# Kernel optimization log

Measured on AMD Instinct MI355X. Metric: run time of the kernel, lower is better.

The kernel has to match this reference:

```python
import jax, jax.numpy as jnp
import numpy as np
import math

EMBED = 1024
HEADS = 16
B, S = 2, 1024

def setup_inputs() -> dict:
    key = jax.random.key(0)
    ks = jax.random.split(key, 6)
    sc = 1.0 / math.sqrt(EMBED)
    return {
        "x": jax.random.normal(ks[0], (B, S, EMBED), dtype=jnp.float32),
        "Wq": jax.random.normal(ks[1], (EMBED, EMBED), dtype=jnp.float32) * sc,
        "Wk": jax.random.normal(ks[2], (EMBED, EMBED), dtype=jnp.float32) * sc,
        "Wv": jax.random.normal(ks[3], (EMBED, EMBED), dtype=jnp.float32) * sc,
        "Wo": jax.random.normal(ks[4], (EMBED, EMBED), dtype=jnp.float32) * sc,
        "bo": jax.random.normal(ks[5], (EMBED,), dtype=jnp.float32) * sc,
        "heads": HEADS,
    }

def reference(x, Wq, Wk, Wv, Wo, bo, heads):
    nB, nS, nE = x.shape
    nH = heads
    nG = nE // nH  # effective number of 'heads' in this (quirky) module

    def split(W):
        # (B,S,E) -> (B,S,G,H) -> (B,G,S,H); per-head dim is nH (as in source)
        return (x @ W).reshape(nB, nS, nG, nH).transpose(0, 2, 1, 3)

    q, k, v = split(Wq), split(Wk), split(Wv)
    # scale uses k.size(-1) == heads, matching the source
    att = jnp.einsum('bgsh,bgth->bgst', q, k) / math.sqrt(nH)
    causal = jnp.tril(jnp.ones((nS, nS), dtype=bool))  # True = keep
    att = jnp.where(causal, att, -jnp.inf)
    att = jax.nn.softmax(att, axis=-1)
    y = jnp.einsum('bgst,bgth->bgsh', att, v)
    y = y.transpose(0, 2, 1, 3).reshape(nB, nS, nE)
    return y @ Wo + bo
```

## Files before the change

### kernel.cpp

```cpp
#include <hip/hip_runtime.h>
#include <hip/hip_bf16.h>
#include <stdint.h>

typedef __attribute__((ext_vector_type(8))) short bf16x8;
typedef __attribute__((ext_vector_type(4))) short bf16x4;
typedef __attribute__((ext_vector_type(4))) float f32x4;

#define NB 2
#define SEQ 1024
#define EMB 1024
#define NH 16
#define NG 64

#if defined(__has_builtin)
#if __has_builtin(__builtin_amdgcn_mfma_f32_16x16x16bf16_1k)
#define QK_1K 1
#else
#define QK_1K 0
#endif
#if __has_builtin(__builtin_amdgcn_exp2f)
#define EXP2(x) __builtin_amdgcn_exp2f(x)
#else
#define EXP2(x) exp2f(x)
#endif
#if __has_builtin(__builtin_amdgcn_rcpf)
#define RCP(x) __builtin_amdgcn_rcpf(x)
#else
#define RCP(x) (1.0f / (x))
#endif
#else
#define QK_1K 0
#define EXP2(x) exp2f(x)
#define RCP(x) (1.0f / (x))
#endif

__device__ __forceinline__ unsigned short f2bf(float f){
  uint32_t u = __float_as_uint(f);
  uint32_t r = (u + 0x7fffu + ((u >> 16) & 1u)) >> 16;
  return (unsigned short)r;
}

__device__ __forceinline__ uint32_t pack_bf2(float lo, float hi){
  uint32_t a = (__float_as_uint(lo) + 0x8000u) >> 16;
  uint32_t b = (__float_as_uint(hi) + 0x8000u) & 0xffff0000u;
  return a | b;
}

__device__ __forceinline__ void gld_lds16(const void* g, void* l){
  __builtin_amdgcn_global_load_lds((__attribute__((address_space(1))) void*)(uintptr_t)(g),
                                   (__attribute__((address_space(3))) void*)(l),
                                   16, 0, 0);
}


__global__ __launch_bounds__(256) void prep_kernel(
    const float* __restrict__ x,
    const float* __restrict__ W0, const float* __restrict__ W1,
    const float* __restrict__ W2, const float* __restrict__ W3,
    unsigned short* __restrict__ xb,
    unsigned short* __restrict__ wtAll)
{
  const int bid = blockIdx.x;
  if (bid < 2048){
    int i = (bid * 256 + threadIdx.x) * 4;
    float4 f = *(const float4*)(x + i);
    ushort4 o;
    o.x = f2bf(f.x); o.y = f2bf(f.y); o.z = f2bf(f.z); o.w = f2bf(f.w);
    *(ushort4*)(xb + i) = o;
    return;
  }
  __shared__ float tile[32][33];
  const int b2 = bid - 2048;
  const int z = b2 & 3;
  const int rest = b2 >> 2;
  const float* W = (z == 0) ? W0 : (z == 1) ? W1 : (z == 2) ? W2 : W3;
  unsigned short* o = wtAll + (size_t)z * EMB * EMB;
  const int n0 = (rest & 31) * 32, k0 = (rest >> 5) * 32;
  const int tx = threadIdx.x & 31, ty = threadIdx.x >> 5;
#pragma unroll
  for (int i = 0; i < 4; i++)
    tile[ty + 8*i][tx] = W[(size_t)(k0 + ty + 8*i) * EMB + n0 + tx];
  __syncthreads();
#pragma unroll
  for (int i = 0; i < 4; i++)
    o[(size_t)(n0 + ty + 8*i) * EMB + k0 + tx] = f2bf(tile[tx][ty + 8*i]);
}


template<int J>
__device__ __forceinline__ void stage_tile(const unsigned short* __restrict__ src,
                                           unsigned short* __restrict__ dst,
                                           int row0, int k0, int t){
#pragma unroll
  for (int j = 0; j < J; ++j){
    const int c = t + 256 * j;
    const int row = c >> 3;
    const int col8 = (c & 7) ^ (row & 7);
    gld_lds16(src + (size_t)(row0 + row) * 1024 + k0 + col8 * 8, dst + c * 8);
  }
}


__global__ __launch_bounds__(256) void gemm_qkv_kernel(
    const unsigned short* __restrict__ A,
    const unsigned short* __restrict__ WtAll,
    unsigned short* __restrict__ qws,
    unsigned short* __restrict__ kws,
    unsigned short* __restrict__ vws)
{
  __shared__ unsigned short As[2][128][64];
  __shared__ unsigned short Bs[2][64][64];
  const int z = blockIdx.z;
  const unsigned short* Bp = WtAll + (size_t)z * EMB * EMB;
  const int m0 = blockIdx.x * 128, n0 = blockIdx.y * 64;
  const int t = threadIdx.x;
  const int l = t & 63, w = t >> 6;
  const int wr = w >> 1, wc = w & 1;
  const int lr = l & 15, lk = l >> 4;
  const int sw0 = (lk ^ (lr & 7)) * 8;
  const int sw1 = ((lk + 4) ^ (lr & 7)) * 8;

  f32x4 acc[4][2];
#pragma unroll
  for (int m = 0; m < 4; m++)
#pragma unroll
    for (int n = 0; n < 2; n++)
#pragma unroll
      for (int r = 0; r < 4; r++) acc[m][n][r] = 0.f;

  stage_tile<4>(A, &As[0][0][0], m0, 0, t);
  stage_tile<2>(Bp, &Bs[0][0][0], n0, 0, t);
  __syncthreads();
  int cur = 0;
  for (int kt = 0; kt < 16; ++kt){
    if (kt < 15){
      stage_tile<4>(A, &As[cur ^ 1][0][0], m0, (kt + 1) * 64, t);
      stage_tile<2>(Bp, &Bs[cur ^ 1][0][0], n0, (kt + 1) * 64, t);
    }
#pragma unroll
    for (int half = 0; half < 2; ++half){
      const int sw = half ? sw1 : sw0;
      bf16x8 af[4], bfr[2];
#pragma unroll
      for (int m = 0; m < 4; m++) af[m]  = *(const bf16x8*)(&As[cur][wr*64 + m*16 + lr][sw]);
#pragma unroll
      for (int n = 0; n < 2; n++) bfr[n] = *(const bf16x8*)(&Bs[cur][wc*32 + n*16 + lr][sw]);
#pragma unroll
      for (int m = 0; m < 4; m++)
#pragma unroll
        for (int n = 0; n < 2; n++)
          acc[m][n] = __builtin_amdgcn_mfma_f32_16x16x32_bf16(af[m], bfr[n], acc[m][n], 0, 0, 0);
    }
    __syncthreads();
    cur ^= 1;
  }

#pragma unroll
  for (int m = 0; m < 4; m++){
    const int rowb = m0 + wr*64 + m*16 + lk*4;
#pragma unroll
    for (int n = 0; n < 2; n++){
      const int col = n0 + wc*32 + n*16 + lr;
      const int g = col >> 4, h = col & 15;
#pragma unroll
      for (int r = 0; r < 4; r++){
        const int rr = rowb + r;
        const int b = rr >> 10, s = rr & 1023;
        const int bg = b * NG + g;
        const float v = acc[m][n][r];
        if (z == 0)      qws[((size_t)bg * 1024 + s) * 16 + h] = f2bf(v * 0.36067376022f);
        else if (z == 1) kws[((size_t)bg * 1024 + s) * 16 + h] = f2bf(v);
        else             vws[((size_t)bg * 16 + h) * 1024 + s] = f2bf(v);
      }
    }
  }
}


__global__ __launch_bounds__(256) void gemm_out_kernel(
    const unsigned short* __restrict__ A,
    const unsigned short* __restrict__ Bw,
    const float* __restrict__ bo,
    float* __restrict__ out)
{
  __shared__ unsigned short As[2][64][64];
  __shared__ unsigned short Bs[2][64][64];
  const int m0 = blockIdx.x * 64, n0 = blockIdx.y * 64;
  const int t = threadIdx.x;
  const int l = t & 63, w = t >> 6;
  const int wr = w >> 1, wc = w & 1;
  const int lr = l & 15, lk = l >> 4;
  const int sw0 = (lk ^ (lr & 7)) * 8;
  const int sw1 = ((lk + 4) ^ (lr & 7)) * 8;

  f32x4 acc[2][2];
#pragma unroll
  for (int m = 0; m < 2; m++)
#pragma unroll
    for (int n = 0; n < 2; n++)
#pragma unroll
      for (int r = 0; r < 4; r++) acc[m][n][r] = 0.f;

  stage_tile<2>(A, &As[0][0][0], m0, 0, t);
  stage_tile<2>(Bw, &Bs[0][0][0], n0, 0, t);
  __syncthreads();
  int cur = 0;
  for (int kt = 0; kt < 16; ++kt){
    if (kt < 15){
      stage_tile<2>(A, &As[cur ^ 1][0][0], m0, (kt + 1) * 64, t);
      stage_tile<2>(Bw, &Bs[cur ^ 1][0][0], n0, (kt + 1) * 64, t);
    }
#pragma unroll
    for (int half = 0; half < 2; ++half){
      const int sw = half ? sw1 : sw0;
      bf16x8 af[2], bfr[2];
#pragma unroll
      for (int m = 0; m < 2; m++) af[m]  = *(const bf16x8*)(&As[cur][wr*32 + m*16 + lr][sw]);
#pragma unroll
      for (int n = 0; n < 2; n++) bfr[n] = *(const bf16x8*)(&Bs[cur][wc*32 + n*16 + lr][sw]);
#pragma unroll
      for (int m = 0; m < 2; m++)
#pragma unroll
        for (int n = 0; n < 2; n++)
          acc[m][n] = __builtin_amdgcn_mfma_f32_16x16x32_bf16(af[m], bfr[n], acc[m][n], 0, 0, 0);
    }
    __syncthreads();
    cur ^= 1;
  }

#pragma unroll
  for (int m = 0; m < 2; m++){
    const int rowb = m0 + wr*32 + m*16 + lk*4;
#pragma unroll
    for (int n = 0; n < 2; n++){
      const int col = n0 + wc*32 + n*16 + lr;
      const float bb = bo[col];
#pragma unroll
      for (int r = 0; r < 4; r++)
        out[(size_t)(rowb + r) * 1024 + col] = acc[m][n][r] + bb;
    }
  }
}


#if QK_1K
struct KF { bf16x4 f[4]; };
#else
struct KF { bf16x8 f[4]; };
#endif

__device__ __forceinline__ void attn_tile(
    const unsigned short* __restrict__ kb,
    const unsigned short* __restrict__ vb,
#if QK_1K
    const bf16x4& aq,
#else
    const bf16x8& aq8,
#endif
    KF& kc, KF& kn,
    f32x4& yacc0, f32x4& yacc1, f32x4& sfr0, f32x4& sfr1,
    unsigned short (*pw)[72],
    int c0, int nt, int tt, int lr, int lk, const bf16x8& bone)
{
  const int t0 = tt << 6;
  if (tt + 1 < nt){
    const int t1 = t0 + 64;
#pragma unroll
    for (int ts = 0; ts < 4; ++ts){
#if QK_1K
      kn.f[ts] = *(const bf16x4*)(kb + (size_t)(t1 + ts*16 + lr) * 16 + lk * 4);
#else
      if (lk < 2) kn.f[ts] = *(const bf16x8*)(kb + (size_t)(t1 + ts*16 + lr) * 16 + lk * 8);
#endif
    }
  }
  const bf16x8 bv0 = *(const bf16x8*)(vb + (size_t)lr * 1024 + t0 + lk * 8);
  const bf16x8 bv1 = *(const bf16x8*)(vb + (size_t)lr * 1024 + t0 + 32 + lk * 8);

  f32x4 sacc[4];
#pragma unroll
  for (int ts = 0; ts < 4; ++ts){
    f32x4 zc;
#pragma unroll
    for (int r = 0; r < 4; r++) zc[r] = 0.f;
#if QK_1K
    sacc[ts] = __builtin_amdgcn_mfma_f32_16x16x16bf16_1k(kc.f[ts], aq, zc, 0, 0, 0);
#else
    sacc[ts] = __builtin_amdgcn_mfma_f32_16x16x32_bf16(kc.f[ts], aq8, zc, 0, 0, 0);
#endif
  }

  if (tt == nt - 1){
    const int qrow = c0 + lr;
#pragma unroll
    for (int ts = 0; ts < 4; ++ts){
      const int key0 = t0 + ts*16 + lk*4;
#pragma unroll
      for (int r = 0; r < 4; ++r)
        if (key0 + r > qrow) sacc[ts][r] = -1e30f;
    }
  }

#pragma unroll
  for (int ts = 0; ts < 4; ++ts){
    const float e0 = EXP2(sacc[ts][0]);
    const float e1 = EXP2(sacc[ts][1]);
    const float e2 = EXP2(sacc[ts][2]);
    const float e3 = EXP2(sacc[ts][3]);
    uint2 u; u.x = pack_bf2(e0, e1); u.y = pack_bf2(e2, e3);
    *(uint2*)(&pw[lr][ts*16 + lk*4]) = u;
  }

  const bf16x8 ap0 = *(const bf16x8*)(&pw[lr][lk * 8]);
  const bf16x8 ap1 = *(const bf16x8*)(&pw[lr][32 + lk * 8]);

  sfr0  = __builtin_amdgcn_mfma_f32_16x16x32_bf16(ap0, bone,  sfr0, 0, 0, 0);
  sfr1  = __builtin_amdgcn_mfma_f32_16x16x32_bf16(ap1, bone,  sfr1, 0, 0, 0);
  yacc0 = __builtin_amdgcn_mfma_f32_16x16x32_bf16(ap0, bv0, yacc0, 0, 0, 0);
  yacc1 = __builtin_amdgcn_mfma_f32_16x16x32_bf16(ap1, bv1, yacc1, 0, 0, 0);

  kc = kn;
}

__global__ __launch_bounds__(256, 4) void attn_kernel(
    const unsigned short* __restrict__ q,
    const unsigned short* __restrict__ k,
    const unsigned short* __restrict__ vt,
    unsigned short* __restrict__ y)
{
  const int blk = blockIdx.x;
  const int bg = blk & 127;
  const int pg = blk >> 7;
  const int t = threadIdx.x, w = t >> 6, l = t & 63;
  const int lr = l & 15, lk = l >> 4;
  const int wvv = 31 - (pg * 4 + w);
  const int cA = 2 * wvv, cB = cA + 1;
  const int c0A = cA * 16, c0B = cB * 16;
  const int ntA = (cA >> 2) + 1, ntB = (cB >> 2) + 1;

  __shared__ unsigned short p_lds[8][16][72];
  unsigned short (*pwA)[72] = p_lds[w * 2];
  unsigned short (*pwB)[72] = p_lds[w * 2 + 1];

  const unsigned short* qb = q + (size_t)bg * 1024 * 16;
  const unsigned short* kb = k + (size_t)bg * 1024 * 16;
  const unsigned short* vb = vt + (size_t)bg * 16 * 1024;
  const int b = bg >> 6, g = bg & 63;

  bf16x8 bone;
#pragma unroll
  for (int i = 0; i < 8; i++) bone[i] = (short)0x3F80;

#if QK_1K
  const bf16x4 aqA = *(const bf16x4*)(qb + (size_t)(c0A + lr) * 16 + lk * 4);
  const bf16x4 aqB = *(const bf16x4*)(qb + (size_t)(c0B + lr) * 16 + lk * 4);
#else
  bf16x8 aqA, aqB;
#pragma unroll
  for (int i = 0; i < 8; i++){ aqA[i] = 0; aqB[i] = 0; }
  if (lk < 2){
    aqA = *(const bf16x8*)(qb + (size_t)(c0A + lr) * 16 + lk * 8);
    aqB = *(const bf16x8*)(qb + (size_t)(c0B + lr) * 16 + lk * 8);
  }
#endif

  f32x4 yA0, yA1, sA0, sA1, yB0, yB1, sB0, sB1;
#pragma unroll
  for (int r = 0; r < 4; r++){
    yA0[r] = yA1[r] = sA0[r] = sA1[r] = 0.f;
    yB0[r] = yB1[r] = sB0[r] = sB1[r] = 0.f;
  }

  KF kcA, knA, kcB, knB;
#if !QK_1K
#pragma unroll
  for (int ts = 0; ts < 4; ++ts)
#pragma unroll
    for (int i = 0; i < 8; i++){ kcA.f[ts][i] = 0; knA.f[ts][i] = 0; kcB.f[ts][i] = 0; knB.f[ts][i] = 0; }
#endif
#pragma unroll
  for (int ts = 0; ts < 4; ++ts){
#if QK_1K
    kcA.f[ts] = *(const bf16x4*)(kb + (size_t)(ts*16 + lr) * 16 + lk * 4);
#else
    if (lk < 2) kcA.f[ts] = *(const bf16x8*)(kb + (size_t)(ts*16 + lr) * 16 + lk * 8);
#endif
    kcB.f[ts] = kcA.f[ts];
  }

  for (int tt = 0; tt < ntA; ++tt){
#if QK_1K
    attn_tile(kb, vb, aqA, kcA, knA, yA0, yA1, sA0, sA1, pwA, c0A, ntA, tt, lr, lk, bone);
    attn_tile(kb, vb, aqB, kcB, knB, yB0, yB1, sB0, sB1, pwB, c0B, ntB, tt, lr, lk, bone);
#else
    attn_tile(kb, vb, aqA, kcA, knA, yA0, yA1, sA0, sA1, pwA, c0A, ntA, tt, lr, lk, bone);
    attn_tile(kb, vb, aqB, kcB, knB, yB0, yB1, sB0, sB1, pwB, c0B, ntB, tt, lr, lk, bone);
#endif
  }
  for (int tt = ntA; tt < ntB; ++tt){
#if QK_1K
    attn_tile(kb, vb, aqB, kcB, knB, yB0, yB1, sB0, sB1, pwB, c0B, ntB, tt, lr, lk, bone);
#else
    attn_tile(kb, vb, aqB, kcB, knB, yB0, yB1, sB0, sB1, pwB, c0B, ntB, tt, lr, lk, bone);
#endif
  }

#pragma unroll
  for (int r = 0; r < 4; ++r){
    const int sA = c0A + lk*4 + r;
    const float vA = (yA0[r] + yA1[r]) * RCP(sA0[r] + sA1[r]);
    y[((size_t)b * 1024 + sA) * 1024 + g * 16 + lr] = f2bf(vA);
    const int sB = c0B + lk*4 + r;
    const float vB = (yB0[r] + yB1[r]) * RCP(sB0[r] + sB1[r]);
    y[((size_t)b * 1024 + sB) * 1024 + g * 16 + lr] = f2bf(vB);
  }
}


extern "C" void kernel_launch(void* const* d_in, const int* in_sizes, int n_in,
                              void* d_out, int out_size, void* d_ws, size_t ws_size,
                              hipStream_t stream)
{
  const float* x  = (const float*)d_in[0];
  const float* Wq = (const float*)d_in[1];
  const float* Wk = (const float*)d_in[2];
  const float* Wv = (const float*)d_in[3];
  const float* Wo = (const float*)d_in[4];
  const float* bo = (const float*)d_in[5];
  float* out = (float*)d_out;
  char* ws = (char*)d_ws;

  unsigned short* xb  = (unsigned short*)(ws);
  unsigned short* wt  = (unsigned short*)(ws + (4u << 20));
  unsigned short* qws = (unsigned short*)(ws + (12u << 20));
  unsigned short* kws = (unsigned short*)(ws + (16u << 20));
  unsigned short* vws = (unsigned short*)(ws + (20u << 20));
  unsigned short* yws = (unsigned short*)(ws);

  prep_kernel<<<6144, 256, 0, stream>>>(x, Wq, Wk, Wv, Wo, xb, wt);
  gemm_qkv_kernel<<<dim3(16, 16, 3), 256, 0, stream>>>(xb, wt, qws, kws, vws);
  attn_kernel<<<1024, 256, 0, stream>>>(qws, kws, vws, yws);
  gemm_out_kernel<<<dim3(32, 16), 256, 0, stream>>>(yws, wt + (size_t)3 * 1024 * 1024, bo, out);
}
```

Baseline: 73.29 us.

## Store Q/K in natural row layout and share K/V fragments across paired query tiles

The QKV GEMM now writes Q and K in their natural [B*S, E] row-major layout instead of a per-group transposed layout, so those epilogue stores become contiguous along columns. The attention kernel reads Q/K with a row stride of 1024 and merges the two query-row tiles into one loop, so each K and V fragment is loaded once and used for both tiles. Because cA is even and cB = cA+1 give the same tile count, the separate tail loop is dropped. The trade-off is that K loads in attention are strided 32-byte reads across rows rather than dense, which may cost more cache traffic per fragment.

```diff
diff --git a/kernel.cpp b/kernel.cpp
--- a/kernel.cpp
+++ b/kernel.cpp
@@ -104,8 +104,8 @@
 __global__ __launch_bounds__(256) void gemm_qkv_kernel(
     const unsigned short* __restrict__ A,
     const unsigned short* __restrict__ WtAll,
-    unsigned short* __restrict__ qws,
-    unsigned short* __restrict__ kws,
+    unsigned short* __restrict__ qn,
+    unsigned short* __restrict__ knat,
     unsigned short* __restrict__ vws)
 {
   __shared__ unsigned short As[2][128][64];
@@ -161,16 +161,17 @@
 #pragma unroll
     for (int n = 0; n < 2; n++){
       const int col = n0 + wc*32 + n*16 + lr;
-      const int g = col >> 4, h = col & 15;
 #pragma unroll
       for (int r = 0; r < 4; r++){
         const int rr = rowb + r;
-        const int b = rr >> 10, s = rr & 1023;
-        const int bg = b * NG + g;
         const float v = acc[m][n][r];
-        if (z == 0)      qws[((size_t)bg * 1024 + s) * 16 + h] = f2bf(v * 0.36067376022f);
-        else if (z == 1) kws[((size_t)bg * 1024 + s) * 16 + h] = f2bf(v);
-        else             vws[((size_t)bg * 16 + h) * 1024 + s] = f2bf(v);
+        if (z == 0)      qn  [(size_t)rr * 1024 + col] = f2bf(v * 0.36067376022f);
+        else if (z == 1) knat[(size_t)rr * 1024 + col] = f2bf(v);
+        else {
+          const int g = col >> 4, h = col & 15;
+          const int b = rr >> 10, s = rr & 1023;
+          vws[(((size_t)(b * NG + g)) * 16 + h) * 1024 + s] = f2bf(v);
+        }
       }
     }
   }
@@ -249,58 +250,13 @@
 struct KF { bf16x8 f[4]; };
 #endif
 
-__device__ __forceinline__ void attn_tile(
-    const unsigned short* __restrict__ kb,
-    const unsigned short* __restrict__ vb,
-#if QK_1K
-    const bf16x4& aq,
-#else
-    const bf16x8& aq8,
-#endif
-    KF& kc, KF& kn,
-    f32x4& yacc0, f32x4& yacc1, f32x4& sfr0, f32x4& sfr1,
+__device__ __forceinline__ void fin_phase(
+    f32x4* sacc,
     unsigned short (*pw)[72],
-    int c0, int nt, int tt, int lr, int lk, const bf16x8& bone)
-{
-  const int t0 = tt << 6;
-  if (tt + 1 < nt){
-    const int t1 = t0 + 64;
-#pragma unroll
-    for (int ts = 0; ts < 4; ++ts){
-#if QK_1K
-      kn.f[ts] = *(const bf16x4*)(kb + (size_t)(t1 + ts*16 + lr) * 16 + lk * 4);
-#else
-      if (lk < 2) kn.f[ts] = *(const bf16x8*)(kb + (size_t)(t1 + ts*16 + lr) * 16 + lk * 8);
-#endif
-    }
-  }
-  const bf16x8 bv0 = *(const bf16x8*)(vb + (size_t)lr * 1024 + t0 + lk * 8);
-  const bf16x8 bv1 = *(const bf16x8*)(vb + (size_t)lr * 1024 + t0 + 32 + lk * 8);
-
-  f32x4 sacc[4];
-#pragma unroll
-  for (int ts = 0; ts < 4; ++ts){
-    f32x4 zc;
-#pragma unroll
-    for (int r = 0; r < 4; r++) zc[r] = 0.f;
-#if QK_1K
-    sacc[ts] = __builtin_amdgcn_mfma_f32_16x16x16bf16_1k(kc.f[ts], aq, zc, 0, 0, 0);
-#else
-    sacc[ts] = __builtin_amdgcn_mfma_f32_16x16x32_bf16(kc.f[ts], aq8, zc, 0, 0, 0);
-#endif
-  }
-
-  if (tt == nt - 1){
-    const int qrow = c0 + lr;
-#pragma unroll
-    for (int ts = 0; ts < 4; ++ts){
-      const int key0 = t0 + ts*16 + lk*4;
-#pragma unroll
-      for (int r = 0; r < 4; ++r)
-        if (key0 + r > qrow) sacc[ts][r] = -1e30f;
-    }
-  }
-
+    const bf16x8& bone, const bf16x8& bv0, const bf16x8& bv1,
+    f32x4& y0, f32x4& y1, f32x4& s0, f32x4& s1,
+    int lr, int lk)
+{
 #pragma unroll
   for (int ts = 0; ts < 4; ++ts){
     const float e0 = EXP2(sacc[ts][0]);
@@ -310,21 +266,17 @@
     uint2 u; u.x = pack_bf2(e0, e1); u.y = pack_bf2(e2, e3);
     *(uint2*)(&pw[lr][ts*16 + lk*4]) = u;
   }
-
   const bf16x8 ap0 = *(const bf16x8*)(&pw[lr][lk * 8]);
   const bf16x8 ap1 = *(const bf16x8*)(&pw[lr][32 + lk * 8]);
-
-  sfr0  = __builtin_amdgcn_mfma_f32_16x16x32_bf16(ap0, bone,  sfr0, 0, 0, 0);
-  sfr1  = __builtin_amdgcn_mfma_f32_16x16x32_bf16(ap1, bone,  sfr1, 0, 0, 0);
-  yacc0 = __builtin_amdgcn_mfma_f32_16x16x32_bf16(ap0, bv0, yacc0, 0, 0, 0);
-  yacc1 = __builtin_amdgcn_mfma_f32_16x16x32_bf16(ap1, bv1, yacc1, 0, 0, 0);
-
-  kc = kn;
+  s0 = __builtin_amdgcn_mfma_f32_16x16x32_bf16(ap0, bone, s0, 0, 0, 0);
+  s1 = __builtin_amdgcn_mfma_f32_16x16x32_bf16(ap1, bone, s1, 0, 0, 0);
+  y0 = __builtin_amdgcn_mfma_f32_16x16x32_bf16(ap0, bv0,  y0, 0, 0, 0);
+  y1 = __builtin_amdgcn_mfma_f32_16x16x32_bf16(ap1, bv1,  y1, 0, 0, 0);
 }
 
 __global__ __launch_bounds__(256, 4) void attn_kernel(
-    const unsigned short* __restrict__ q,
-    const unsigned short* __restrict__ k,
+    const unsigned short* __restrict__ qn,
+    const unsigned short* __restrict__ knat,
     const unsigned short* __restrict__ vt,
     unsigned short* __restrict__ y)
 {
@@ -334,33 +286,33 @@
   const int t = threadIdx.x, w = t >> 6, l = t & 63;
   const int lr = l & 15, lk = l >> 4;
   const int wvv = 31 - (pg * 4 + w);
-  const int cA = 2 * wvv, cB = cA + 1;
-  const int c0A = cA * 16, c0B = cB * 16;
-  const int ntA = (cA >> 2) + 1, ntB = (cB >> 2) + 1;
+  const int cA = 2 * wvv;
+  const int c0A = cA * 16, c0B = c0A + 16;
+  const int nt = (cA >> 2) + 1;
 
   __shared__ unsigned short p_lds[8][16][72];
   unsigned short (*pwA)[72] = p_lds[w * 2];
   unsigned short (*pwB)[72] = p_lds[w * 2 + 1];
 
-  const unsigned short* qb = q + (size_t)bg * 1024 * 16;
-  const unsigned short* kb = k + (size_t)bg * 1024 * 16;
-  const unsigned short* vb = vt + (size_t)bg * 16 * 1024;
   const int b = bg >> 6, g = bg & 63;
+  const unsigned short* qb = qn   + (size_t)b * 1024 * 1024 + g * 16;
+  const unsigned short* kb = knat + (size_t)b * 1024 * 1024 + g * 16;
+  const unsigned short* vb = vt   + (size_t)bg * 16 * 1024;
 
   bf16x8 bone;
 #pragma unroll
   for (int i = 0; i < 8; i++) bone[i] = (short)0x3F80;
 
 #if QK_1K
-  const bf16x4 aqA = *(const bf16x4*)(qb + (size_t)(c0A + lr) * 16 + lk * 4);
-  const bf16x4 aqB = *(const bf16x4*)(qb + (size_t)(c0B + lr) * 16 + lk * 4);
+  const bf16x4 aqA = *(const bf16x4*)(qb + (size_t)(c0A + lr) * 1024 + lk * 4);
+  const bf16x4 aqB = *(const bf16x4*)(qb + (size_t)(c0B + lr) * 1024 + lk * 4);
 #else
   bf16x8 aqA, aqB;
 #pragma unroll
   for (int i = 0; i < 8; i++){ aqA[i] = 0; aqB[i] = 0; }
   if (lk < 2){
-    aqA = *(const bf16x8*)(qb + (size_t)(c0A + lr) * 16 + lk * 8);
-    aqB = *(const bf16x8*)(qb + (size_t)(c0B + lr) * 16 + lk * 8);
+    aqA = *(const bf16x8*)(qb + (size_t)(c0A + lr) * 1024 + lk * 8);
+    aqB = *(const bf16x8*)(qb + (size_t)(c0B + lr) * 1024 + lk * 8);
   }
 #endif
 
@@ -371,48 +323,90 @@
     yB0[r] = yB1[r] = sB0[r] = sB1[r] = 0.f;
   }
 
-  KF kcA, knA, kcB, knB;
+  KF kc, kn;
 #if !QK_1K
 #pragma unroll
   for (int ts = 0; ts < 4; ++ts)
 #pragma unroll
-    for (int i = 0; i < 8; i++){ kcA.f[ts][i] = 0; knA.f[ts][i] = 0; kcB.f[ts][i] = 0; knB.f[ts][i] = 0; }
+    for (int i = 0; i < 8; i++){ kc.f[ts][i] = 0; kn.f[ts][i] = 0; }
 #endif
 #pragma unroll
   for (int ts = 0; ts < 4; ++ts){
 #if QK_1K
-    kcA.f[ts] = *(const bf16x4*)(kb + (size_t)(ts*16 + lr) * 16 + lk * 4);
-#else
-    if (lk < 2) kcA.f[ts] = *(const bf16x8*)(kb + (size_t)(ts*16 + lr) * 16 + lk * 8);
-#endif
-    kcB.f[ts] = kcA.f[ts];
-  }
-
-  for (int tt = 0; tt < ntA; ++tt){
-#if QK_1K
-    attn_tile(kb, vb, aqA, kcA, knA, yA0, yA1, sA0, sA1, pwA, c0A, ntA, tt, lr, lk, bone);
-    attn_tile(kb, vb, aqB, kcB, knB, yB0, yB1, sB0, sB1, pwB, c0B, ntB, tt, lr, lk, bone);
-#else
-    attn_tile(kb, vb, aqA, kcA, knA, yA0, yA1, sA0, sA1, pwA, c0A, ntA, tt, lr, lk, bone);
-    attn_tile(kb, vb, aqB, kcB, knB, yB0, yB1, sB0, sB1, pwB, c0B, ntB, tt, lr, lk, bone);
-#endif
-  }
-  for (int tt = ntA; tt < ntB; ++tt){
-#if QK_1K
-    attn_tile(kb, vb, aqB, kcB, knB, yB0, yB1, sB0, sB1, pwB, c0B, ntB, tt, lr, lk, bone);
-#else
-    attn_tile(kb, vb, aqB, kcB, knB, yB0, yB1, sB0, sB1, pwB, c0B, ntB, tt, lr, lk, bone);
-#endif
+    kc.f[ts] = *(const bf16x4*)(kb + (size_t)(ts*16 + lr) * 1024 + lk * 4);
+#else
+    if (lk < 2) kc.f[ts] = *(const bf16x8*)(kb + (size_t)(ts*16 + lr) * 1024 + lk * 8);
+#endif
+  }
+
+  for (int tt = 0; tt < nt; ++tt){
+    const int t0 = tt << 6;
+
+    if (tt + 1 < nt){
+      const int t1 = t0 + 64;
+#pragma unroll
+      for (int ts = 0; ts < 4; ++ts){
+#if QK_1K
+        kn.f[ts] = *(const bf16x4*)(kb + (size_t)(t1 + ts*16 + lr) * 1024 + lk * 4);
+#else
+        if (lk < 2) kn.f[ts] = *(const bf16x8*)(kb + (size_t)(t1 + ts*16 + lr) * 1024 + lk * 8);
+#endif
+      }
+    }
+    const bf16x8 bv0 = *(const bf16x8*)(vb + (size_t)lr * 1024 + t0 + lk * 8);
+    const bf16x8 bv1 = *(const bf16x8*)(vb + (size_t)lr * 1024 + t0 + 32 + lk * 8);
+
+    f32x4 sA[4], sB[4];
+#pragma unroll
+    for (int ts = 0; ts < 4; ++ts){
+      f32x4 zc;
+#pragma unroll
+      for (int r = 0; r < 4; r++) zc[r] = 0.f;
+#if QK_1K
+      sA[ts] = __builtin_amdgcn_mfma_f32_16x16x16bf16_1k(kc.f[ts], aqA, zc, 0, 0, 0);
+#else
+      sA[ts] = __builtin_amdgcn_mfma_f32_16x16x32_bf16(kc.f[ts], aqA, zc, 0, 0, 0);
+#endif
+    }
+#pragma unroll
+    for (int ts = 0; ts < 4; ++ts){
+      f32x4 zc;
+#pragma unroll
+      for (int r = 0; r < 4; r++) zc[r] = 0.f;
+#if QK_1K
+      sB[ts] = __builtin_amdgcn_mfma_f32_16x16x16bf16_1k(kc.f[ts], aqB, zc, 0, 0, 0);
+#else
+      sB[ts] = __builtin_amdgcn_mfma_f32_16x16x32_bf16(kc.f[ts], aqB, zc, 0, 0, 0);
+#endif
+    }
+
+    if (tt == nt - 1){
+      const int qrA = c0A + lr, qrB = c0B + lr;
+#pragma unroll
+      for (int ts = 0; ts < 4; ++ts){
+        const int key0 = t0 + ts*16 + lk*4;
+#pragma unroll
+        for (int r = 0; r < 4; ++r){
+          if (key0 + r > qrA) sA[ts][r] = -1e30f;
+          if (key0 + r > qrB) sB[ts][r] = -1e30f;
+        }
+      }
+    }
+
+    fin_phase(sA, pwA, bone, bv0, bv1, yA0, yA1, sA0, sA1, lr, lk);
+    fin_phase(sB, pwB, bone, bv0, bv1, yB0, yB1, sB0, sB1, lr, lk);
+
+    kc = kn;
   }
 
 #pragma unroll
   for (int r = 0; r < 4; ++r){
-    const int sA = c0A + lk*4 + r;
+    const int sAi = c0A + lk*4 + r;
     const float vA = (yA0[r] + yA1[r]) * RCP(sA0[r] + sA1[r]);
-    y[((size_t)b * 1024 + sA) * 1024 + g * 16 + lr] = f2bf(vA);
-    const int sB = c0B + lk*4 + r;
+    y[((size_t)b * 1024 + sAi) * 1024 + g * 16 + lr] = f2bf(vA);
+    const int sBi = c0B + lk*4 + r;
     const float vB = (yB0[r] + yB1[r]) * RCP(sB0[r] + sB1[r]);
-    y[((size_t)b * 1024 + sB) * 1024 + g * 16 + lr] = f2bf(vB);
+    y[((size_t)b * 1024 + sBi) * 1024 + g * 16 + lr] = f2bf(vB);
   }
 }
 
@@ -430,15 +424,15 @@
   float* out = (float*)d_out;
   char* ws = (char*)d_ws;
 
-  unsigned short* xb  = (unsigned short*)(ws);
-  unsigned short* wt  = (unsigned short*)(ws + (4u << 20));
-  unsigned short* qws = (unsigned short*)(ws + (12u << 20));
-  unsigned short* kws = (unsigned short*)(ws + (16u << 20));
-  unsigned short* vws = (unsigned short*)(ws + (20u << 20));
-  unsigned short* yws = (unsigned short*)(ws);
+  unsigned short* xb   = (unsigned short*)(ws);
+  unsigned short* wt   = (unsigned short*)(ws + (4u << 20));
+  unsigned short* qn   = (unsigned short*)(ws + (12u << 20));
+  unsigned short* knat = (unsigned short*)(ws + (16u << 20));
+  unsigned short* vws  = (unsigned short*)(ws + (20u << 20));
+  unsigned short* yws  = (unsigned short*)(ws);
 
   prep_kernel<<<6144, 256, 0, stream>>>(x, Wq, Wk, Wv, Wo, xb, wt);
-  gemm_qkv_kernel<<<dim3(16, 16, 3), 256, 0, stream>>>(xb, wt, qws, kws, vws);
-  attn_kernel<<<1024, 256, 0, stream>>>(qws, kws, vws, yws);
+  gemm_qkv_kernel<<<dim3(16, 16, 3), 256, 0, stream>>>(xb, wt, qn, knat, vws);
+  attn_kernel<<<1024, 256, 0, stream>>>(qn, knat, vws, yws);
   gemm_out_kernel<<<dim3(32, 16), 256, 0, stream>>>(yws, wt + (size_t)3 * 1024 * 1024, bo, out);
 }
```

New measurement: 81.62 us. 11.4% more time.
